# Performance work log

Hardware: AMD Instinct MI355X
Metric: run time of the kernel (lower is better)

The kernel has to match this reference:

```python
import jax, jax.numpy as jnp
import numpy as np
import math

B, S, DIM = 2, 2048, 2048
NH = 16
HD = DIM // NH  # 128
RANK = 32


def setup_inputs() -> dict:
    key = jax.random.key(0)
    ks = jax.random.split(key, 10)
    x = jax.random.normal(ks[0], (B, S, DIM), dtype=jnp.float32)
    # causal additive mask (use -1e9 instead of -inf for grad-safety)
    mask = jnp.where(jnp.tril(jnp.ones((S, S), dtype=bool)), 0.0, -1e9).astype(jnp.float32)[None, None]
    # rotary frequencies, as in llama: theta = 10000^{-2i/d}
    inv_freq = 1.0 / (10000.0 ** (jnp.arange(0, HD, 2, dtype=jnp.float32) / HD))  # [HD/2]
    t = jnp.arange(S, dtype=jnp.float32)
    freqs = jnp.outer(t, inv_freq)  # [S, HD/2]
    freqs_cos = jnp.cos(freqs)
    freqs_sin = jnp.sin(freqs)
    scale = 0.02
    wq = jax.random.normal(ks[1], (DIM, DIM), dtype=jnp.float32) * scale
    wk = jax.random.normal(ks[2], (DIM, DIM), dtype=jnp.float32) * scale
    wv = jax.random.normal(ks[3], (DIM, DIM), dtype=jnp.float32) * scale
    wo = jax.random.normal(ks[4], (DIM, DIM), dtype=jnp.float32) * scale
    wa_q = jax.random.normal(ks[5], (RANK, DIM), dtype=jnp.float32) * 0.02
    wa_k = jax.random.normal(ks[6], (RANK, DIM), dtype=jnp.float32) * 0.02
    return {"x": x, "mask": mask, "freqs_cos": freqs_cos, "freqs_sin": freqs_sin,
            "wq": wq, "wk": wk, "wv": wv, "wo": wo, "wa_q": wa_q, "wa_k": wa_k}


def _apply_rope(t, cos, sin):
    # t: [B, S, H, HD]; cos/sin: [S, HD/2]
    tr = t.reshape(*t.shape[:-1], HD // 2, 2)
    tre, tim = tr[..., 0], tr[..., 1]
    c = cos[None, :, None, :]
    s = sin[None, :, None, :]
    out_re = tre * c - tim * s
    out_im = tre * s + tim * c
    return jnp.stack([out_re, out_im], axis=-1).reshape(t.shape)


def reference(x, mask, freqs_cos, freqs_sin, wq, wk, wv, wo, wa_q, wa_k):
    bsz, seqlen, dim = x.shape
    xq = (x @ wq.T).reshape(bsz, seqlen, NH, HD)
    xk = (x @ wk.T).reshape(bsz, seqlen, NH, HD)
    xv = (x @ wv.T).reshape(bsz, seqlen, NH, HD)
    # low-rank adaptive gate (computed on detached x in the original)
    xd = jax.lax.stop_gradient(x)
    xq_h = xd @ wa_q.T  # [B, S, 32]
    xk_h = xd @ wa_k.T  # [B, S, 32]
    adaptive_mask = jnp.einsum('bqr,bkr->bqk', xq_h, xk_h)  # [B, S, S]

    xq = _apply_rope(xq, freqs_cos, freqs_sin)
    xk = _apply_rope(xk, freqs_cos, freqs_sin)

    q = xq.transpose(0, 2, 1, 3)  # [B, H, S, HD]
    k = xk.transpose(0, 2, 1, 3)
    v = xv.transpose(0, 2, 1, 3)

    scores = jnp.einsum('bhqd,bhkd->bhqk', q, k) / math.sqrt(HD)
    scores = scores + mask
    scores = jax.nn.softmax(scores.astype(jnp.float32), axis=-1).astype(q.dtype)
    scores = scores * jax.nn.sigmoid(adaptive_mask)[:, None]  # gate, broadcast over heads
    out = jnp.einsum('bhqk,bhkd->bhqd', scores, v)
    out = out.transpose(0, 2, 1, 3).reshape(bsz, seqlen, -1)
    return out @ wo.T
```

## Files before the change

kernel.cpp:

```cpp
#include <hip/hip_runtime.h>

typedef __attribute__((ext_vector_type(8))) short short8v;
typedef __attribute__((ext_vector_type(4))) short short4v;
typedef __attribute__((ext_vector_type(4))) float floatx4;

#define S_    2048
#define DIM_  2048
#define NW_   6272

#define ASG(p) ((__attribute__((address_space(1))) void*)(p))
#define ASL(p) ((__attribute__((address_space(3))) void*)(p))

__device__ __forceinline__ short f2bf(float f){
  union { float f; unsigned u; } c; c.f = f;
  unsigned u = c.u;
  unsigned r = (u + 0x7fffu + ((u >> 16) & 1u)) >> 16;
  return (short)r;
}
__device__ __forceinline__ float bf2f(short s){
  union { unsigned u; float f; } c; c.u = ((unsigned)(unsigned short)s) << 16;
  return c.f;
}

__global__ __launch_bounds__(256) void cvt_k(const float* __restrict__ in,
                                             short* __restrict__ out, int n){
  int i = blockIdx.x*256 + threadIdx.x;
  int idx = i*4;
  if (idx >= n) return;
  floatx4 v = *(const floatx4*)(in + idx);
  short4v o;
  o[0]=f2bf(v[0]); o[1]=f2bf(v[1]); o[2]=f2bf(v[2]); o[3]=f2bf(v[3]);
  *(short4v*)(out + idx) = o;
}

__global__ __launch_bounds__(256)
void cvt_w(const float* wq, const float* waq, const float* wak,
           const float* wk, const float* wv, const float* wo,
           short* Wcat, short* wob){
  const float* src; short* dst; int n;
  switch (blockIdx.y){
    case 0: src=wq;  dst=Wcat;                 n=4194304; break;
    case 1: src=waq; dst=Wcat+(size_t)2048*2048; n=65536; break;
    case 2: src=wak; dst=Wcat+(size_t)2080*2048; n=65536; break;
    case 3: src=wk;  dst=Wcat+(size_t)2112*2048; n=4194304; break;
    case 4: src=wv;  dst=Wcat+(size_t)4224*2048; n=4194304; break;
    case 5: src=wo;  dst=wob;                  n=4194304; break;
    default: {
      int idx = (blockIdx.x*256 + threadIdx.x)*4;
      if (idx < 131072){
        short4v z = {0,0,0,0};
        *(short4v*)(Wcat + (size_t)4160*2048 + idx) = z;
      }
      return;
    }
  }
  int idx = (blockIdx.x*256 + threadIdx.x)*4;
  if (idx >= n) return;
  floatx4 v = *(const floatx4*)(src + idx);
  short4v o;
  o[0]=f2bf(v[0]); o[1]=f2bf(v[1]); o[2]=f2bf(v[2]); o[3]=f2bf(v[3]);
  *(short4v*)(dst + idx) = o;
}

__global__ __launch_bounds__(256,4)
void gemm_qkv(const short* __restrict__ A, const short* __restrict__ B,
              short* __restrict__ Cout, short* __restrict__ Vt){
  __shared__ short SH[2][128][64];
  short (*As)[64] = SH[0];
  short (*Bs)[64] = SH[1];
  const int K = 2048, N = NW_;
  int tid = threadIdx.x;
  int wave = tid>>6, lane = tid&63, quad = lane>>4, l16 = lane&15;
  int l7 = l16&7;
  int m0 = blockIdx.x*128, n0 = blockIdx.y*128;
  int wm = (wave>>1)*64, wn = (wave&1)*64;
  floatx4 acc[4][4] = {};

  int lr = lane>>3;
  int sw = (lane&7) ^ lr;
  const short* Abase = A + (size_t)(m0 + wave*32 + lr)*K + sw*8;
  const short* Bbase = B + (size_t)(n0 + wave*32 + lr)*K + sw*8;

  for (int k0 = 0; k0 < K; k0 += 64){
    __syncthreads();
    #pragma unroll
    for (int i=0;i<4;i++){
      __builtin_amdgcn_global_load_lds(ASG(Abase + (size_t)(i*8)*K + k0),
                                       ASL(&As[wave*32 + i*8][0]), 16, 0, 0);
      __builtin_amdgcn_global_load_lds(ASG(Bbase + (size_t)(i*8)*K + k0),
                                       ASL(&Bs[wave*32 + i*8][0]), 16, 0, 0);
    }
    __syncthreads();
    #pragma unroll
    for (int ks=0; ks<2; ks++){
      short8v af[4], bf[4];
      #pragma unroll
      for (int i=0;i<4;i++) af[i] = *(short8v*)&As[wm + i*16 + l16][((ks*4+quad)^l7)*8];
      #pragma unroll
      for (int j=0;j<4;j++) bf[j] = *(short8v*)&Bs[wn + j*16 + l16][((ks*4+quad)^l7)*8];
      #pragma unroll
      for (int i=0;i<4;i++)
        #pragma unroll
        for (int j=0;j<4;j++)
          acc[i][j] = __builtin_amdgcn_mfma_f32_16x16x32_bf16(af[i], bf[j], acc[i][j], 0,0,0);
    }
  }

  if (n0 < 4224){
    #pragma unroll
    for (int i=0;i<4;i++)
      #pragma unroll
      for (int r=0;r<4;r++){
        int gm = m0 + wm + i*16 + quad*4 + r;
        #pragma unroll
        for (int j=0;j<4;j++){
          int gn = n0 + wn + j*16 + l16;
          Cout[(size_t)gm*N + gn] = f2bf(acc[i][j][r]);
        }
      }
  } else {
    short* T = &SH[0][0][0];
    __syncthreads();
    #pragma unroll
    for (int i=0;i<4;i++){
      int mb = wm + i*16 + quad*4;
      int mc = mb>>3, mi = mb&7;
      #pragma unroll
      for (int j=0;j<4;j++){
        int n = wn + j*16 + l16;
        short4v p;
        p[0]=f2bf(acc[i][j][0]); p[1]=f2bf(acc[i][j][1]);
        p[2]=f2bf(acc[i][j][2]); p[3]=f2bf(acc[i][j][3]);
        *(short4v*)&T[n*128 + ((mc ^ (n&7))*8) + mi] = p;
      }
    }
    __syncthreads();
    int nl = tid>>1, half = tid&1;
    #pragma unroll
    for (int c=0;c<8;c++){
      int cc = half*8 + c;
      short8v v = *(short8v*)&T[nl*128 + ((cc ^ (nl&7))*8)];
      *(short8v*)&Vt[(size_t)(n0 - 4224 + nl)*4096 + m0 + cc*8] = v;
    }
  }
}

__global__ __launch_bounds__(256,2)
void gemm_nt_f32(const short* __restrict__ A, const short* __restrict__ B,
                 float* __restrict__ Cout, int M, int N, int K){
  __shared__ short As[128][64];
  __shared__ short Bs[128][64];
  int tid = threadIdx.x;
  int wave = tid>>6, lane = tid&63, quad = lane>>4, l16 = lane&15;
  int l7 = l16&7;
  int m0 = blockIdx.x*128, n0 = blockIdx.y*128;
  int wm = (wave>>1)*64, wn = (wave&1)*64;
  floatx4 acc[4][4] = {};

  int lr = lane>>3;
  int sw = (lane&7) ^ lr;
  const short* Abase = A + (size_t)(m0 + wave*32 + lr)*K + sw*8;
  const short* Bbase = B + (size_t)(n0 + wave*32 + lr)*K + sw*8;

  for (int k0 = 0; k0 < K; k0 += 64){
    __syncthreads();
    #pragma unroll
    for (int i=0;i<4;i++){
      __builtin_amdgcn_global_load_lds(ASG(Abase + (size_t)(i*8)*K + k0),
                                       ASL(&As[wave*32 + i*8][0]), 16, 0, 0);
      __builtin_amdgcn_global_load_lds(ASG(Bbase + (size_t)(i*8)*K + k0),
                                       ASL(&Bs[wave*32 + i*8][0]), 16, 0, 0);
    }
    __syncthreads();
    #pragma unroll
    for (int ks=0; ks<2; ks++){
      short8v af[4], bf[4];
      #pragma unroll
      for (int i=0;i<4;i++) af[i] = *(short8v*)&As[wm + i*16 + l16][((ks*4+quad)^l7)*8];
      #pragma unroll
      for (int j=0;j<4;j++) bf[j] = *(short8v*)&Bs[wn + j*16 + l16][((ks*4+quad)^l7)*8];
      #pragma unroll
      for (int i=0;i<4;i++)
        #pragma unroll
        for (int j=0;j<4;j++)
          acc[i][j] = __builtin_amdgcn_mfma_f32_16x16x32_bf16(af[i], bf[j], acc[i][j], 0,0,0);
    }
  }
  #pragma unroll
  for (int i=0;i<4;i++)
    #pragma unroll
    for (int r=0;r<4;r++){
      int gm = m0 + wm + i*16 + quad*4 + r;
      #pragma unroll
      for (int j=0;j<4;j++){
        int gn = n0 + wn + j*16 + l16;
        Cout[(size_t)gm*N + gn] = acc[i][j][r];
      }
    }
}

__global__ __launch_bounds__(256) void rope_k(short* __restrict__ X,
                                              const float* __restrict__ fcos,
                                              const float* __restrict__ fsin){
  int i = blockIdx.x*256 + threadIdx.x;
  int row = i >> 10;
  int p = i & 1023;
  int s = row & (S_-1);
  int pp = p & 63;
  float c = fcos[s*64+pp], sn = fsin[s*64+pp];
  size_t a = (size_t)row*NW_ + 2112 + p*2;
  int v = *(int*)(X + a);
  float re = bf2f((short)(v & 0xffff)), im = bf2f((short)(v >> 16));
  float orr = re*c - im*sn, oi = re*sn + im*c;
  *(int*)(X + a) = ((int)(unsigned short)f2bf(oi) << 16) | (unsigned short)f2bf(orr);
}

__global__ __launch_bounds__(256)
void gate_k(const short* __restrict__ X, short* __restrict__ G){
  int kt = blockIdx.x, qt = blockIdx.y, b = blockIdx.z;
  if (kt > qt) return;
  int tid = threadIdx.x, wave = tid>>6, lane = tid&63, quad = lane>>4, l16 = lane&15;
  const float NL2E = -1.44269504f;

  short8v qh = *(const short8v*)&X[(size_t)(b*2048 + qt*64 + wave*16 + l16)*NW_ + 2048 + quad*8];
  floatx4 am[4];
  #pragma unroll
  for (int j=0;j<4;j++){
    short8v kh = *(const short8v*)&X[(size_t)(b*2048 + kt*64 + j*16 + l16)*NW_ + 2080 + quad*8];
    floatx4 z = {0.f,0.f,0.f,0.f};
    am[j] = __builtin_amdgcn_mfma_f32_16x16x32_bf16(qh, kh, z, 0,0,0);
  }
  short* Gd = G + (((size_t)(b*32 + kt)*2048) + qt*64 + wave*16 + quad*4)*64 + l16*4;
  #pragma unroll
  for (int r=0;r<4;r++){
    short4v sv;
    #pragma unroll
    for (int j=0;j<4;j++){
      float g = __builtin_amdgcn_rcpf(1.f + __builtin_amdgcn_exp2f(am[j][r]*NL2E));
      sv[j] = f2bf(g);
    }
    *(short4v*)(Gd + (size_t)r*64) = sv;
  }
}

__global__ __launch_bounds__(256,2)
void flash_k(const short* __restrict__ Qc, const short* __restrict__ Vt,
             const short* __restrict__ G, const float* __restrict__ fcos,
             const float* __restrict__ fsin, short* __restrict__ O){
  int pi = blockIdx.x, h = blockIdx.y, b = blockIdx.z;
  int tid = threadIdx.x, wave = tid>>6, lane = tid&63, quad = lane>>4, l16 = lane&15;
  int l7 = l16&7;

  __shared__ short Ks [2][64][128];
  __shared__ short Vts[2][128][64];
  __shared__ short Ps [4][16][72];

  const float CS = 1.44269504f * 0.08838834764831845f;

  auto stage = [&](int kt, int buf){
    int k0 = kt*64;
    const short* Ksrc = Qc + ((size_t)(b*2048 + k0 + wave*16))*NW_ + 2112 + h*128;
    int r4 = lane>>4, c16 = lane&15;
    #pragma unroll
    for (int j=0;j<4;j++)
      __builtin_amdgcn_global_load_lds(
        ASG(Ksrc + (size_t)(j*4 + r4)*NW_ + ((c16 ^ r4 ^ ((j&1)*4))*8)),
        ASL(&Ks[buf][wave*16 + j*4][0]), 16, 0, 0);
    const short* Vsrc = Vt + ((size_t)(h*128 + wave*32 + (lane>>3)))*4096 + b*2048 + k0
                        + (((lane&7) ^ (lane>>3))*8);
    #pragma unroll
    for (int j=0;j<4;j++)
      __builtin_amdgcn_global_load_lds(
        ASG(Vsrc + (size_t)(j*8)*4096),
        ASL(&Vts[buf][wave*32 + j*8][0]), 16, 0, 0);
  };

  for (int ph = 0; ph < 2; ph++){
    int qt = ph ? pi : 31 - pi;
    size_t qrow = (size_t)(b*2048 + qt*64 + wave*16 + l16);
    int srow = qt*64 + wave*16 + l16;
    short8v qf[4];
    #pragma unroll
    for (int ks=0;ks<4;ks++)
      qf[ks] = *(const short8v*)&Qc[qrow*NW_ + h*128 + ks*32 + quad*8];
    #pragma unroll
    for (int ks=0;ks<4;ks++)
      #pragma unroll
      for (int jj=0;jj<4;jj++){
        float re = bf2f(qf[ks][2*jj]), im = bf2f(qf[ks][2*jj+1]);
        int p = ks*16 + quad*4 + jj;
        float c = fcos[srow*64 + p], sn = fsin[srow*64 + p];
        qf[ks][2*jj]   = f2bf(re*c - im*sn);
        qf[ks][2*jj+1] = f2bf(re*sn + im*c);
      }

    floatx4 oacc[8] = {};
    float lp[4] = {0.f,0.f,0.f,0.f};

    __syncthreads();
    stage(0, 0);
    for (int kt=0; kt<=qt; kt++){
      __syncthreads();
      if (kt < qt) stage(kt+1, (kt+1)&1);
      int bc = kt&1;

      const short* gb = G + (((size_t)(b*32 + kt)*2048) + qt*64 + wave*16 + quad*4)*64 + l16*4;
      short4v g4[4];
      #pragma unroll
      for (int r=0;r<4;r++) g4[r] = *(const short4v*)(gb + (size_t)r*64);

      floatx4 sacc[4] = {};
      #pragma unroll
      for (int j=0;j<4;j++)
        #pragma unroll
        for (int ks2=0;ks2<4;ks2++){
          short8v kf = *(short8v*)&Ks[bc][j*16+l16][((ks2*4+quad)^l7)*8];
          sacc[j] = __builtin_amdgcn_mfma_f32_16x16x32_bf16(qf[ks2], kf, sacc[j], 0,0,0);
        }

      bool diag = (kt == qt);
      int qin = wave*16 + quad*4;
      #pragma unroll
      for (int j=0;j<4;j++){
        int kin = j*16 + l16;
        #pragma unroll
        for (int r=0;r<4;r++){
          bool keep = !diag || (kin <= qin + r);
          float p = keep ? __builtin_amdgcn_exp2f(sacc[j][r]*CS) : 0.f;
          lp[r] += p;
          Ps[wave][quad*4+r][j*16+l16] = f2bf(p * bf2f(g4[r][j]));
        }
      }
      #pragma unroll
      for (int ks2=0; ks2<2; ks2++){
        short8v pf = *(short8v*)&Ps[wave][l16][ks2*32 + quad*8];
        #pragma unroll
        for (int dt=0; dt<8; dt++){
          short8v vf = *(short8v*)&Vts[bc][dt*16 + l16][((ks2*4+quad)^l7)*8];
          oacc[dt] = __builtin_amdgcn_mfma_f32_16x16x32_bf16(pf, vf, oacc[dt], 0,0,0);
        }
      }
    }

    #pragma unroll
    for (int r=0;r<4;r++)
      #pragma unroll
      for (int off=1; off<16; off<<=1)
        lp[r] += __shfl_xor(lp[r], off, 64);
    #pragma unroll
    for (int r=0;r<4;r++){
      float inv = __builtin_amdgcn_rcpf(lp[r]);
      size_t orow = (size_t)(b*2048 + qt*64 + wave*16 + quad*4 + r);
      #pragma unroll
      for (int dt=0;dt<8;dt++)
        O[orow*2048 + h*128 + dt*16 + l16] = f2bf(oacc[dt][r]*inv);
    }
  }
}

extern "C" void kernel_launch(void* const* d_in, const int* in_sizes, int n_in,
                              void* d_out, int out_size, void* d_ws, size_t ws_size,
                              hipStream_t stream){
  const float* x    = (const float*)d_in[0];
  const float* fcos = (const float*)d_in[2];
  const float* fsin = (const float*)d_in[3];
  const float* wq   = (const float*)d_in[4];
  const float* wk   = (const float*)d_in[5];
  const float* wv   = (const float*)d_in[6];
  const float* wo   = (const float*)d_in[7];
  const float* waq  = (const float*)d_in[8];
  const float* wak  = (const float*)d_in[9];
  float* out = (float*)d_out;

  char* ws = (char*)d_ws;
  size_t off = 0;
  short* xb   = (short*)(ws + off); off += (size_t)4096*2048*2;
  short* Wcat = (short*)(ws + off); off += (size_t)NW_*2048*2;
  short* wob  = (short*)(ws + off); off += (size_t)2048*2048*2;
  short* XQKV = (short*)(ws + off); off += (size_t)4096*NW_*2;
  short* Vtb  = (short*)(ws + off); off += (size_t)2048*4096*2;
  short* G    = xb;
  short* Ob   = Wcat;

  cvt_k<<<8192,256,0,stream>>>(x, xb, 8388608);
  cvt_w<<<dim3(4096,7),256,0,stream>>>(wq, waq, wak, wk, wv, wo, Wcat, wob);

  gemm_qkv<<<dim3(32,49),256,0,stream>>>(xb, Wcat, XQKV, Vtb);

  rope_k<<<16384,256,0,stream>>>(XQKV, fcos, fsin);
  gate_k<<<dim3(32,32,2),256,0,stream>>>(XQKV, G);

  flash_k<<<dim3(16,16,2),256,0,stream>>>(XQKV, Vtb, G, fcos, fsin, Ob);

  gemm_nt_f32<<<dim3(32,16),256,0,stream>>>(Ob, wob, out, 4096, 2048, 2048);
}
```

Measured before the change: 422.6 us.

## Enlarge flash attention query tile to 128 rows per block for K/V reuse

The flash kernel now processes 128 query rows per block: each wave handles two 16-row subtiles that share every staged K and V tile. This halves the number of blocks and the global-to-LDS traffic per query, at the cost of twice the accumulator registers, so the occupancy hint drops to 1. Waves whose rows lie entirely before a key tile skip that tile's compute, and the causal mask is now checked per wave range. Separately, the grid order puts heads on x, and the output GEMM's launch bound is raised to 4 blocks per CU.

After: 428.0 us. Within noise of the previous version (+1.3%).

```diff
diff --git a/kernel.cpp b/kernel.cpp
--- a/kernel.cpp
+++ b/kernel.cpp
@@ -145,7 +145,7 @@
   }
 }
 
-__global__ __launch_bounds__(256,2)
+__global__ __launch_bounds__(256,4)
 void gemm_nt_f32(const short* __restrict__ A, const short* __restrict__ B,
                  float* __restrict__ Cout, int M, int N, int K){
   __shared__ short As[128][64];
@@ -243,17 +243,17 @@
   }
 }
 
-__global__ __launch_bounds__(256,2)
+__global__ __launch_bounds__(256,1)
 void flash_k(const short* __restrict__ Qc, const short* __restrict__ Vt,
              const short* __restrict__ G, const float* __restrict__ fcos,
              const float* __restrict__ fsin, short* __restrict__ O){
-  int pi = blockIdx.x, h = blockIdx.y, b = blockIdx.z;
+  int h = blockIdx.x, pi = blockIdx.y, b = blockIdx.z;
   int tid = threadIdx.x, wave = tid>>6, lane = tid&63, quad = lane>>4, l16 = lane&15;
   int l7 = l16&7;
 
   __shared__ short Ks [2][64][128];
   __shared__ short Vts[2][128][64];
-  __shared__ short Ps [4][16][72];
+  __shared__ short Ps [4][2][16][72];
 
   const float CS = 1.44269504f * 0.08838834764831845f;
 
@@ -276,84 +276,100 @@
   };
 
   for (int ph = 0; ph < 2; ph++){
-    int qt = ph ? pi : 31 - pi;
-    size_t qrow = (size_t)(b*2048 + qt*64 + wave*16 + l16);
-    int srow = qt*64 + wave*16 + l16;
-    short8v qf[4];
-    #pragma unroll
-    for (int ks=0;ks<4;ks++)
-      qf[ks] = *(const short8v*)&Qc[qrow*NW_ + h*128 + ks*32 + quad*8];
-    #pragma unroll
-    for (int ks=0;ks<4;ks++)
-      #pragma unroll
-      for (int jj=0;jj<4;jj++){
-        float re = bf2f(qf[ks][2*jj]), im = bf2f(qf[ks][2*jj+1]);
-        int p = ks*16 + quad*4 + jj;
-        float c = fcos[srow*64 + p], sn = fsin[srow*64 + p];
-        qf[ks][2*jj]   = f2bf(re*c - im*sn);
-        qf[ks][2*jj+1] = f2bf(re*sn + im*c);
-      }
-
-    floatx4 oacc[8] = {};
-    float lp[4] = {0.f,0.f,0.f,0.f};
+    int qt = ph ? pi : 15 - pi;
+    int qmin0 = qt*128 + wave*32;
+    short8v qf[2][4];
+    #pragma unroll
+    for (int i=0;i<2;i++){
+      int srow = qmin0 + i*16 + l16;
+      size_t qrow = (size_t)(b*2048 + srow);
+      #pragma unroll
+      for (int ks=0;ks<4;ks++)
+        qf[i][ks] = *(const short8v*)&Qc[qrow*NW_ + h*128 + ks*32 + quad*8];
+      #pragma unroll
+      for (int ks=0;ks<4;ks++)
+        #pragma unroll
+        for (int jj=0;jj<4;jj++){
+          float re = bf2f(qf[i][ks][2*jj]), im = bf2f(qf[i][ks][2*jj+1]);
+          int p = ks*16 + quad*4 + jj;
+          float c = fcos[srow*64 + p], sn = fsin[srow*64 + p];
+          qf[i][ks][2*jj]   = f2bf(re*c - im*sn);
+          qf[i][ks][2*jj+1] = f2bf(re*sn + im*c);
+        }
+    }
+
+    floatx4 oacc[2][8] = {};
+    float lp[2][4] = {{0.f,0.f,0.f,0.f},{0.f,0.f,0.f,0.f}};
+    int KT = 2*qt + 2;
 
     __syncthreads();
     stage(0, 0);
-    for (int kt=0; kt<=qt; kt++){
+    for (int kt=0; kt<KT; kt++){
       __syncthreads();
-      if (kt < qt) stage(kt+1, (kt+1)&1);
-      int bc = kt&1;
-
-      const short* gb = G + (((size_t)(b*32 + kt)*2048) + qt*64 + wave*16 + quad*4)*64 + l16*4;
-      short4v g4[4];
-      #pragma unroll
-      for (int r=0;r<4;r++) g4[r] = *(const short4v*)(gb + (size_t)r*64);
-
-      floatx4 sacc[4] = {};
+      if (kt+1 < KT) stage(kt+1, (kt+1)&1);
+      int bc = kt&1, k0 = kt*64;
+
+      if (k0 > qmin0 + 15) continue;
+
+      floatx4 sacc[2][4] = {};
       #pragma unroll
       for (int j=0;j<4;j++)
         #pragma unroll
         for (int ks2=0;ks2<4;ks2++){
           short8v kf = *(short8v*)&Ks[bc][j*16+l16][((ks2*4+quad)^l7)*8];
-          sacc[j] = __builtin_amdgcn_mfma_f32_16x16x32_bf16(qf[ks2], kf, sacc[j], 0,0,0);
+          sacc[0][j] = __builtin_amdgcn_mfma_f32_16x16x32_bf16(qf[0][ks2], kf, sacc[0][j], 0,0,0);
+          sacc[1][j] = __builtin_amdgcn_mfma_f32_16x16x32_bf16(qf[1][ks2], kf, sacc[1][j], 0,0,0);
         }
 
-      bool diag = (kt == qt);
-      int qin = wave*16 + quad*4;
-      #pragma unroll
-      for (int j=0;j<4;j++){
-        int kin = j*16 + l16;
-        #pragma unroll
-        for (int r=0;r<4;r++){
-          bool keep = !diag || (kin <= qin + r);
-          float p = keep ? __builtin_amdgcn_exp2f(sacc[j][r]*CS) : 0.f;
-          lp[r] += p;
-          Ps[wave][quad*4+r][j*16+l16] = f2bf(p * bf2f(g4[r][j]));
+      bool need_mask = (k0 + 63 > qmin0);
+      #pragma unroll
+      for (int i=0;i<2;i++){
+        const short* gb = G + (((size_t)(b*32 + kt)*2048) + qmin0 + i*16 + quad*4)*64 + l16*4;
+        short4v g4[4];
+        #pragma unroll
+        for (int r=0;r<4;r++) g4[r] = *(const short4v*)(gb + (size_t)r*64);
+        int qbase = qmin0 + i*16 + quad*4;
+        #pragma unroll
+        for (int j=0;j<4;j++){
+          int kin = k0 + j*16 + l16;
+          #pragma unroll
+          for (int r=0;r<4;r++){
+            bool keep = !need_mask || (kin <= qbase + r);
+            float p = keep ? __builtin_amdgcn_exp2f(sacc[i][j][r]*CS) : 0.f;
+            lp[i][r] += p;
+            Ps[wave][i][quad*4+r][j*16+l16] = f2bf(p * bf2f(g4[r][j]));
+          }
         }
       }
+
       #pragma unroll
       for (int ks2=0; ks2<2; ks2++){
-        short8v pf = *(short8v*)&Ps[wave][l16][ks2*32 + quad*8];
+        short8v pf0 = *(short8v*)&Ps[wave][0][l16][ks2*32 + quad*8];
+        short8v pf1 = *(short8v*)&Ps[wave][1][l16][ks2*32 + quad*8];
         #pragma unroll
         for (int dt=0; dt<8; dt++){
           short8v vf = *(short8v*)&Vts[bc][dt*16 + l16][((ks2*4+quad)^l7)*8];
-          oacc[dt] = __builtin_amdgcn_mfma_f32_16x16x32_bf16(pf, vf, oacc[dt], 0,0,0);
+          oacc[0][dt] = __builtin_amdgcn_mfma_f32_16x16x32_bf16(pf0, vf, oacc[0][dt], 0,0,0);
+          oacc[1][dt] = __builtin_amdgcn_mfma_f32_16x16x32_bf16(pf1, vf, oacc[1][dt], 0,0,0);
         }
       }
     }
 
     #pragma unroll
-    for (int r=0;r<4;r++)
-      #pragma unroll
-      for (int off=1; off<16; off<<=1)
-        lp[r] += __shfl_xor(lp[r], off, 64);
-    #pragma unroll
-    for (int r=0;r<4;r++){
-      float inv = __builtin_amdgcn_rcpf(lp[r]);
-      size_t orow = (size_t)(b*2048 + qt*64 + wave*16 + quad*4 + r);
-      #pragma unroll
-      for (int dt=0;dt<8;dt++)
-        O[orow*2048 + h*128 + dt*16 + l16] = f2bf(oacc[dt][r]*inv);
+    for (int i=0;i<2;i++){
+      #pragma unroll
+      for (int r=0;r<4;r++)
+        #pragma unroll
+        for (int off=1; off<16; off<<=1)
+          lp[i][r] += __shfl_xor(lp[i][r], off, 64);
+      #pragma unroll
+      for (int r=0;r<4;r++){
+        float inv = __builtin_amdgcn_rcpf(lp[i][r]);
+        size_t orow = (size_t)(b*2048 + qmin0 + i*16 + quad*4 + r);
+        #pragma unroll
+        for (int dt=0;dt<8;dt++)
+          O[orow*2048 + h*128 + dt*16 + l16] = f2bf(oacc[i][dt][r]*inv);
+      }
     }
   }
 }
@@ -390,7 +406,7 @@
   rope_k<<<16384,256,0,stream>>>(XQKV, fcos, fsin);
   gate_k<<<dim3(32,32,2),256,0,stream>>>(XQKV, G);
 
-  flash_k<<<dim3(16,16,2),256,0,stream>>>(XQKV, Vtb, G, fcos, fsin, Ob);
+  flash_k<<<dim3(16,8,2),256,0,stream>>>(XQKV, Vtb, G, fcos, fsin, Ob);
 
   gemm_nt_f32<<<dim3(32,16),256,0,stream>>>(Ob, wob, out, 4096, 2048, 2048);
 }
```
